# Performance work log

Measured on AMD Instinct MI355X. Metric: run time of the kernel, lower is better.

Reference implementation:

```python
import jax, jax.numpy as jnp
import numpy as np
import math

N_HEAD = 16
N_KV_HEAD = 4
N_EMBED = 2048
HEAD_DIM = N_EMBED // N_HEAD  # 128
ROPE_BASE = 10000.0


def _rope_tables(T, dim, dtype):
    inv_freq = 1.0 / (ROPE_BASE ** (jnp.arange(0, dim, 2, dtype=jnp.float32) / dim))
    t = jnp.arange(T, dtype=jnp.float32)
    freqs = jnp.outer(t, inv_freq)            # (T, dim/2)
    emb = jnp.concatenate([freqs, freqs], -1) # (T, dim)
    return jnp.cos(emb).astype(dtype), jnp.sin(emb).astype(dtype)


def _rotate_half(x):
    half = x.shape[-1] // 2
    return jnp.concatenate([-x[..., half:], x[..., :half]], axis=-1)


def setup_inputs() -> dict:
    key = jax.random.key(0)
    kx, kq, kk, kv, ko = jax.random.split(key, 5)
    B, T, C = 2, 2048, N_EMBED
    s = 0.02
    return {
        "x": jax.random.normal(kx, (B, T, C), jnp.float32),
        "Wq": jax.random.normal(kq, (N_HEAD * HEAD_DIM, C), jnp.float32) * s,
        "Wk": jax.random.normal(kk, (N_KV_HEAD * HEAD_DIM, C), jnp.float32) * s,
        "Wv": jax.random.normal(kv, (N_KV_HEAD * HEAD_DIM, C), jnp.float32) * s,
        "Wo": jax.random.normal(ko, (C, N_HEAD * HEAD_DIM), jnp.float32) * s,
    }


def reference(x, Wq, Wk, Wv, Wo):
    B, T, C = x.shape
    H, KV, D = N_HEAD, N_KV_HEAD, HEAD_DIM
    rep = H // KV

    q = jnp.einsum('btc,oc->bto', x, Wq).reshape(B, T, H, D).transpose(0, 2, 1, 3)   # (B,H,T,D)
    k = jnp.einsum('btc,oc->bto', x, Wk).reshape(B, T, KV, D).transpose(0, 2, 1, 3)  # (B,KV,T,D)
    v = jnp.einsum('btc,oc->bto', x, Wv).reshape(B, T, KV, D).transpose(0, 2, 1, 3)

    cos, sin = _rope_tables(T, D, x.dtype)  # (T,D) broadcast over (B,h,T,D)
    q = q * cos + _rotate_half(q) * sin
    k = k * cos + _rotate_half(k) * sin

    # GQA: head h attends to kv head h // rep (== repeat_interleave in torch).
    qg = q.reshape(B, KV, rep, T, D)
    scale = 1.0 / math.sqrt(D)
    attn = jnp.einsum('bgrtd,bgsd->bgrts', qg, k) * scale  # (B,KV,rep,T,T)
    causal = jnp.tril(jnp.ones((T, T), dtype=bool))
    attn = jnp.where(causal, attn, -jnp.inf)
    attn = jax.nn.softmax(attn, axis=-1)
    out = jnp.einsum('bgrts,bgsd->bgrtd', attn, v)          # (B,KV,rep,T,D)
    out = out.reshape(B, H, T, D).transpose(0, 2, 1, 3).reshape(B, T, H * D)
    return jnp.einsum('bto,co->btc', out, Wo)
```

## Files before the change

### kernel.cpp

```cpp
#include <hip/hip_runtime.h>
#include <stdint.h>

typedef unsigned short u16;
typedef __attribute__((ext_vector_type(8))) short short8;
typedef __attribute__((ext_vector_type(4))) short short4v;
typedef __attribute__((ext_vector_type(4))) float f32x4;

#define NB_  2
#define NT_  2048
#define NC_  2048
#define NH_  16
#define NKV_ 4
#define HD_  128
#define NM_  (NB_*NT_)
#define NQKV 3072

__device__ __forceinline__ u16 f2b(float x) {
  uint32_t u = __float_as_uint(x);
  u += 0x7fffu + ((u >> 16) & 1u);
  return (u16)(u >> 16);
}
__device__ __forceinline__ float b2f(u16 x) {
  return __uint_as_float(((uint32_t)x) << 16);
}
__device__ __forceinline__ uint32_t pk2t(float a, float b) {
  return (__float_as_uint(a) >> 16) | (__float_as_uint(b) & 0xFFFF0000u);
}

typedef __attribute__((address_space(1))) uint32_t* gp1_t;
typedef __attribute__((address_space(3))) uint32_t* lp3_t;
__device__ __forceinline__ void async_ld16(const void* g, void* l) {
  __builtin_amdgcn_global_load_lds((gp1_t)(uintptr_t)g, (lp3_t)(uintptr_t)l, 16, 0, 0);
}

__global__ void f2bf_all(const float* __restrict__ x,  const float* __restrict__ wq,
                         const float* __restrict__ wk, const float* __restrict__ wv,
                         const float* __restrict__ wo,
                         u16* xb, u16* wqb, u16* wkb, u16* wvb, u16* wob) {
  int bid = blockIdx.x;
  const float* src; u16* dst; int base;
  if      (bid < 8192)  { src = x;  dst = xb;  base = bid; }
  else if (bid < 12288) { src = wq; dst = wqb; base = bid - 8192; }
  else if (bid < 13312) { src = wk; dst = wkb; base = bid - 12288; }
  else if (bid < 14336) { src = wv; dst = wvb; base = bid - 13312; }
  else                  { src = wo; dst = wob; base = bid - 14336; }
  int i = base * 256 + threadIdx.x;
  const float4 v = ((const float4*)src)[i];
  short4v o;
  o[0] = (short)f2b(v.x); o[1] = (short)f2b(v.y);
  o[2] = (short)f2b(v.z); o[3] = (short)f2b(v.w);
  *(short4v*)(dst + (size_t)i * 4) = o;
}

__global__ void postk(const u16* __restrict__ qkv,
                      u16* __restrict__ Qr, u16* __restrict__ Kr, u16* __restrict__ Vt) {
  __shared__ u16 tile[64][72];
  int bid = blockIdx.x;
  if (bid < 20480) {
    u16* out; int nheads; int tid; int coff; float osc;
    if (bid < 16384) { out = Qr; nheads = NH_;  tid = bid * 256 + threadIdx.x; coff = 0;
                       osc = 0.08838834764831845f; }
    else             { out = Kr; nheads = NKV_; tid = (bid - 16384) * 256 + threadIdx.x; coff = 2048;
                       osc = 1.0f; }
    int j = tid & 63;
    int t = (tid >> 6) & (NT_ - 1);
    int bh = tid >> 17;
    int h = bh % nheads, b = bh / nheads;
    const u16* src = qkv + ((size_t)(b * NT_ + t)) * NQKV + coff + h * HD_;
    float q0 = b2f(src[j]), q1 = b2f(src[j + 64]);
    float inv = expf(-0.14391156831212787f * (float)j);
    float ang = (float)t * inv;
    float c = cosf(ang), s = sinf(ang);
    u16* dst = out + ((size_t)(b * nheads + h) * NT_ + t) * HD_;
    dst[j]      = f2b((q0 * c - q1 * s) * osc);
    dst[j + 64] = f2b((q1 * c + q0 * s) * osc);
  } else {
    int idx = bid - 20480;
    int tt = idx & 63, dd = idx >> 6;
    int tid = threadIdx.x;
    int r = tid >> 3, c8 = (tid & 7) * 8;
#pragma unroll
    for (int it = 0; it < 2; ++it) {
      int row = r + it * 32;
      short8 v = *(const short8*)(qkv + (size_t)(tt * 64 + row) * NQKV + 2560 + dd * 64 + c8);
      *(short8*)(&tile[row][c8]) = v;
    }
    __syncthreads();
    int b = (tt * 64) >> 11, t0 = (tt * 64) & (NT_ - 1);
    int dl = tid >> 3, t8 = (tid & 7) * 8;
#pragma unroll
    for (int it = 0; it < 2; ++it) {
      int d = dl + it * 32;
      int gcol = dd * 64 + d;
      int kv = gcol >> 7, drow = gcol & 127;
      short8 v;
#pragma unroll
      for (int k = 0; k < 8; ++k) v[k] = (short)tile[t8 + k][d];
      *(short8*)(Vt + ((size_t)(b * NKV_ + kv) * HD_ + drow) * NT_ + t0 + t8) = v;
    }
  }
}

__global__ __launch_bounds__(256, 2)
void gemm192(const u16* __restrict__ A, const u16* __restrict__ B, u16* __restrict__ C, int K)
{
  __shared__ u16 As[2 * 128 * 32];
  __shared__ u16 Bs[2 * 192 * 32];
  const int bx = blockIdx.x, by = blockIdx.y;
  const int m0 = by * 128, n0 = bx * 192;
  const int tid = threadIdx.x;
  const int wave = tid >> 6, lane = tid & 63;
  const int quad = lane >> 4, l15 = lane & 15;
  const int wm = wave >> 1, wn = wave & 1;

  const int p_local = lane >> 3;
  const int s7 = lane & 7;
  const int mlo = s7 >> 2;
  const int gg = (s7 & 3) ^ (p_local & 3);
  const int rowc = p_local * 2 + mlo;
  const int kel = gg * 8;

  const u16* Ag[2]; u16* Al[2];
#pragma unroll
  for (int q = 0; q < 2; ++q) {
    const int c = wave * 2 + q;
    Ag[q] = A + (size_t)(m0 + c * 16 + rowc) * K + kel;
    Al[q] = As + c * 512;
  }
  const u16* Bg[3]; u16* Bl[3];
#pragma unroll
  for (int q = 0; q < 3; ++q) {
    const int c = wave * 3 + q;
    Bg[q] = B + (size_t)(n0 + c * 16 + rowc) * K + kel;
    Bl[q] = Bs + c * 512;
  }

  f32x4 acc[4][6] = {};

  int a_addr[4], b_addr[6];
#pragma unroll
  for (int i = 0; i < 4; ++i) {
    int m = wm * 64 + i * 16 + l15;
    a_addr[i] = ((m >> 1) * 8 + (m & 1) * 4 + (quad ^ ((m >> 1) & 3))) * 8;
  }
#pragma unroll
  for (int i = 0; i < 6; ++i) {
    int n = wn * 96 + i * 16 + l15;
    b_addr[i] = ((n >> 1) * 8 + (n & 1) * 4 + (quad ^ ((n >> 1) & 3))) * 8;
  }

  const int nk = K >> 5;
#pragma unroll
  for (int q = 0; q < 2; ++q) async_ld16(Ag[q], Al[q]);
#pragma unroll
  for (int q = 0; q < 3; ++q) async_ld16(Bg[q], Bl[q]);

  for (int i = 0; i < nk; ++i) {
    __syncthreads();
    if (i + 1 < nk) {
      const int offA = ((i + 1) & 1) * 4096;
      const int offB = ((i + 1) & 1) * 6144;
      const int k0 = (i + 1) << 5;
#pragma unroll
      for (int q = 0; q < 2; ++q) async_ld16(Ag[q] + k0, Al[q] + offA);
#pragma unroll
      for (int q = 0; q < 3; ++q) async_ld16(Bg[q] + k0, Bl[q] + offB);
    }
    const int offA = (i & 1) * 4096;
    const int offB = (i & 1) * 6144;
    short8 af[4], bf[6];
#pragma unroll
    for (int j = 0; j < 4; ++j) af[j] = *(const short8*)(As + offA + a_addr[j]);
#pragma unroll
    for (int j = 0; j < 6; ++j) bf[j] = *(const short8*)(Bs + offB + b_addr[j]);
#pragma unroll
    for (int mb = 0; mb < 4; ++mb)
#pragma unroll
      for (int nb = 0; nb < 6; ++nb)
        acc[mb][nb] = __builtin_amdgcn_mfma_f32_16x16x32_bf16(af[mb], bf[nb], acc[mb][nb], 0, 0, 0);
  }

#pragma unroll
  for (int mb = 0; mb < 4; ++mb)
#pragma unroll
    for (int nb = 0; nb < 6; ++nb) {
      const int gn = n0 + wn * 96 + nb * 16 + l15;
#pragma unroll
      for (int r = 0; r < 4; ++r) {
        const int gm = m0 + wm * 64 + mb * 16 + quad * 4 + r;
        C[(size_t)gm * NQKV + gn] = f2b(acc[mb][nb][r]);
      }
    }
}

__global__ __launch_bounds__(256, 2)
void gemm128o(const u16* __restrict__ A, const u16* __restrict__ B, float* __restrict__ C, int K)
{
  __shared__ u16 As[2 * 128 * 32];
  __shared__ u16 Bs[2 * 128 * 32];
  const int bx = blockIdx.x, by = blockIdx.y;
  const int m0 = by * 128, n0 = bx * 128;
  const int tid = threadIdx.x;
  const int wave = tid >> 6, lane = tid & 63;
  const int quad = lane >> 4, l15 = lane & 15;
  const int wm = wave >> 1, wn = wave & 1;

  const int p_local = lane >> 3;
  const int s7 = lane & 7;
  const int mlo = s7 >> 2;
  const int gg = (s7 & 3) ^ (p_local & 3);
  const int rowc = p_local * 2 + mlo;
  const int kel = gg * 8;

  const u16* Ag[2]; const u16* Bg[2];
  u16* Al[2]; u16* Bl[2];
#pragma unroll
  for (int q = 0; q < 2; ++q) {
    const int c = wave * 2 + q;
    Ag[q] = A + (size_t)(m0 + c * 16 + rowc) * K + kel;
    Bg[q] = B + (size_t)(n0 + c * 16 + rowc) * K + kel;
    Al[q] = As + c * 512;
    Bl[q] = Bs + c * 512;
  }

  f32x4 acc[4][4] = {};

  int a_addr[4], b_addr[4];
#pragma unroll
  for (int i = 0; i < 4; ++i) {
    int m = wm * 64 + i * 16 + l15;
    a_addr[i] = ((m >> 1) * 8 + (m & 1) * 4 + (quad ^ ((m >> 1) & 3))) * 8;
    int n = wn * 64 + i * 16 + l15;
    b_addr[i] = ((n >> 1) * 8 + (n & 1) * 4 + (quad ^ ((n >> 1) & 3))) * 8;
  }

  const int nk = K >> 5;
#pragma unroll
  for (int q = 0; q < 2; ++q) {
    async_ld16(Ag[q], Al[q]);
    async_ld16(Bg[q], Bl[q]);
  }

  for (int i = 0; i < nk; ++i) {
    __syncthreads();
    if (i + 1 < nk) {
      const int off = ((i + 1) & 1) * 4096;
      const int k0 = (i + 1) << 5;
#pragma unroll
      for (int q = 0; q < 2; ++q) {
        async_ld16(Ag[q] + k0, Al[q] + off);
        async_ld16(Bg[q] + k0, Bl[q] + off);
      }
    }
    const int off = (i & 1) * 4096;
    short8 af[4], bf[4];
#pragma unroll
    for (int j = 0; j < 4; ++j) af[j] = *(const short8*)(As + off + a_addr[j]);
#pragma unroll
    for (int j = 0; j < 4; ++j) bf[j] = *(const short8*)(Bs + off + b_addr[j]);
#pragma unroll
    for (int mb = 0; mb < 4; ++mb)
#pragma unroll
      for (int nb = 0; nb < 4; ++nb)
        acc[mb][nb] = __builtin_amdgcn_mfma_f32_16x16x32_bf16(af[mb], bf[nb], acc[mb][nb], 0, 0, 0);
  }

#pragma unroll
  for (int mb = 0; mb < 4; ++mb)
#pragma unroll
    for (int nb = 0; nb < 4; ++nb) {
      const int gn = n0 + wn * 64 + nb * 16 + l15;
#pragma unroll
      for (int r = 0; r < 4; ++r) {
        const int gm = m0 + wm * 64 + mb * 16 + quad * 4 + r;
        C[(size_t)gm * NC_ + gn] = acc[mb][nb][r];
      }
    }
}

__global__ __launch_bounds__(256, 2)
void attn_kernel(const u16* __restrict__ Q, const u16* __restrict__ Kg,
                 const u16* __restrict__ Vt, u16* __restrict__ O)
{
  __shared__ u16 Ks[2 * 8192];
  __shared__ u16 Vs[2 * 8192];
  const int bx = blockIdx.x;
  const int h  = blockIdx.y;
  const int b  = blockIdx.z;
  const int qi = b ? (15 - bx) : bx;
  const int kv = h >> 2;
  const int tid = threadIdx.x;
  const int wave = tid >> 6, lane = tid & 63;
  const int quad = lane >> 4, l15 = lane & 15;
  const int qw = qi * 128 + wave * 32;

  const u16* Kbase = Kg + (size_t)(b * NKV_ + kv) * NT_ * HD_;
  const u16* Vbase = Vt + (size_t)(b * NKV_ + kv) * HD_ * NT_;

  short8 qf[2][4];
#pragma unroll
  for (int qs = 0; qs < 2; ++qs) {
    const u16* qb = Q + ((size_t)(b * NH_ + h) * NT_ + qw + qs * 16 + l15) * HD_ + quad * 8;
#pragma unroll
    for (int kb = 0; kb < 4; ++kb) qf[qs][kb] = *(const short8*)(qb + kb * 32);
  }

  const int krow = lane >> 4, kgs = lane & 15;
  const int vrow = lane >> 3, vgs = lane & 7;

  auto stage = [&](int kt, int pbuf) {
    u16* KsB = Ks + pbuf * 8192;
    u16* VsB = Vs + pbuf * 8192;
#pragma unroll
    for (int qq = 0; qq < 4; ++qq) {
      const int c = wave * 4 + qq;
      const int rk = c * 4 + krow;
      const int gk = kgs ^ (rk & 7);
      async_ld16(Kbase + (size_t)(kt * 64 + rk) * HD_ + gk * 8, KsB + c * 512);
      const int rv = c * 8 + vrow;
      const int gv = vgs ^ (rv & 7);
      async_ld16(Vbase + (size_t)rv * NT_ + kt * 64 + gv * 8, VsB + c * 512);
    }
  };

  short8 vone;
#pragma unroll
  for (int j = 0; j < 8; ++j) vone[j] = (short)0x3F80;

  f32x4 acc_o[2][8] = {};
  f32x4 acc_l[2] = {};
  const int nkt = 2 * qi + 2;

  stage(0, 0);

  for (int kt = 0; kt < nkt; ++kt) {
    __syncthreads();
    if (kt + 1 < nkt) stage(kt + 1, (kt + 1) & 1);
    if (kt * 64 > qw + 31) continue;

    const u16* KsB = Ks + (kt & 1) * 8192;
    const u16* VsB = Vs + (kt & 1) * 8192;

    f32x4 S[2][4] = {};
#pragma unroll
    for (int nb = 0; nb < 4; ++nb) {
      const int row = nb * 16 + l15;
#pragma unroll
      for (int kb = 0; kb < 4; ++kb) {
        const int gi = kb * 4 + quad;
        short8 kfr = *(const short8*)(KsB + row * 128 + (gi ^ (row & 7)) * 8);
        S[0][nb] = __builtin_amdgcn_mfma_f32_16x16x32_bf16(kfr, qf[0][kb], S[0][nb], 0, 0, 0);
        S[1][nb] = __builtin_amdgcn_mfma_f32_16x16x32_bf16(kfr, qf[1][kb], S[1][nb], 0, 0, 0);
      }
    }

#pragma unroll
    for (int qs = 0; qs < 2; ++qs) {
      if (kt * 64 + 63 > qw + qs * 16) {
        const int qg = qw + qs * 16 + l15;
#pragma unroll
        for (int nb = 0; nb < 4; ++nb)
#pragma unroll
          for (int r = 0; r < 4; ++r) {
            const int key = kt * 64 + nb * 16 + quad * 4 + r;
            if (key > qg) S[qs][nb][r] = -INFINITY;
          }
      }
    }

#pragma unroll
    for (int qs = 0; qs < 2; ++qs)
#pragma unroll
      for (int nb = 0; nb < 4; ++nb)
#pragma unroll
        for (int r = 0; r < 4; ++r)
          S[qs][nb][r] = __expf(S[qs][nb][r]);

    short8 pf[2][2];
#pragma unroll
    for (int qs = 0; qs < 2; ++qs) {
      uint32_t d0[4], d1[4];
#pragma unroll
      for (int nb = 0; nb < 4; ++nb) {
        d0[nb] = pk2t(S[qs][nb][0], S[qs][nb][1]);
        d1[nb] = pk2t(S[qs][nb][2], S[qs][nb][3]);
      }
      const int srcA = ((quad & 1) * 2) * 16 + l15;
      const int srcB = srcA + 16;
      const bool hi = quad >= 2;
#pragma unroll
      for (int k2 = 0; k2 < 2; ++k2) {
        const int nbL = k2 * 2, nbH = k2 * 2 + 1;
        uint32_t a0 = (uint32_t)__shfl((int)d0[nbL], srcA);
        uint32_t a1 = (uint32_t)__shfl((int)d1[nbL], srcA);
        uint32_t a2 = (uint32_t)__shfl((int)d0[nbL], srcB);
        uint32_t a3 = (uint32_t)__shfl((int)d1[nbL], srcB);
        uint32_t b0 = (uint32_t)__shfl((int)d0[nbH], srcA);
        uint32_t b1 = (uint32_t)__shfl((int)d1[nbH], srcA);
        uint32_t b2 = (uint32_t)__shfl((int)d0[nbH], srcB);
        uint32_t b3 = (uint32_t)__shfl((int)d1[nbH], srcB);
        uint32_t w[4] = { hi ? b0 : a0, hi ? b1 : a1, hi ? b2 : a2, hi ? b3 : a3 };
        pf[qs][k2] = *(short8*)w;
      }
    }

#pragma unroll
    for (int qs = 0; qs < 2; ++qs) {
      acc_l[qs] = __builtin_amdgcn_mfma_f32_16x16x32_bf16(pf[qs][0], vone, acc_l[qs], 0, 0, 0);
      acc_l[qs] = __builtin_amdgcn_mfma_f32_16x16x32_bf16(pf[qs][1], vone, acc_l[qs], 0, 0, 0);
    }

#pragma unroll
    for (int db = 0; db < 8; ++db) {
      const int row = db * 16 + l15;
#pragma unroll
      for (int k2 = 0; k2 < 2; ++k2) {
        const int gi = k2 * 4 + quad;
        short8 vf = *(const short8*)(VsB + row * 64 + (gi ^ (row & 7)) * 8);
        acc_o[0][db] = __builtin_amdgcn_mfma_f32_16x16x32_bf16(pf[0][k2], vf, acc_o[0][db], 0, 0, 0);
        acc_o[1][db] = __builtin_amdgcn_mfma_f32_16x16x32_bf16(pf[1][k2], vf, acc_o[1][db], 0, 0, 0);
      }
    }
  }

#pragma unroll
  for (int qs = 0; qs < 2; ++qs) {
    float inv_r[4];
#pragma unroll
    for (int r = 0; r < 4; ++r) inv_r[r] = 1.f / acc_l[qs][r];
    const size_t orow = ((size_t)b * NT_ + qw + qs * 16) * (NH_ * HD_);
#pragma unroll
    for (int db = 0; db < 8; ++db)
#pragma unroll
      for (int r = 0; r < 4; ++r)
        O[orow + (size_t)(quad * 4 + r) * (NH_ * HD_) + h * HD_ + db * 16 + l15] =
            f2b(acc_o[qs][db][r] * inv_r[r]);
  }
}

extern "C" void kernel_launch(void* const* d_in, const int* in_sizes, int n_in,
                              void* d_out, int out_size, void* d_ws, size_t ws_size,
                              hipStream_t stream) {
  const float* x  = (const float*)d_in[0];
  const float* Wq = (const float*)d_in[1];
  const float* Wk = (const float*)d_in[2];
  const float* Wv = (const float*)d_in[3];
  const float* Wo = (const float*)d_in[4];
  float* out = (float*)d_out;
  char* ws = (char*)d_ws;
  const size_t MB = (size_t)1 << 20;
  u16* xb    = (u16*)(ws + 0);
  u16* wqkv  = (u16*)(ws + 16 * MB);
  u16* wkb   = (u16*)(ws + 24 * MB);
  u16* wvb   = (u16*)(ws + 26 * MB);
  u16* wob   = (u16*)(ws + 28 * MB);
  u16* qkvrw = (u16*)(ws + 36 * MB);
  u16* Qr    = (u16*)(ws + 60 * MB);
  u16* Kr    = (u16*)(ws + 76 * MB);
  u16* Vtb   = (u16*)(ws + 80 * MB);
  u16* Ob    = xb;

  f2bf_all<<<18432, 256, 0, stream>>>(x, Wq, Wk, Wv, Wo, xb, wqkv, wkb, wvb, wob);

  gemm192<<<dim3(16, 32), 256, 0, stream>>>(xb, wqkv, qkvrw, 2048);

  postk<<<20992, 256, 0, stream>>>(qkvrw, Qr, Kr, Vtb);

  attn_kernel<<<dim3(16, 16, 2), 256, 0, stream>>>(Qr, Kr, Vtb, Ob);

  gemm128o<<<dim3(16, 32), 256, 0, stream>>>(Ob, wob, out, 2048);
}
```

Baseline: 283.7 us.

## Split attention work across 8 waves with 16 query rows each

The attention kernel now launches 512 threads per block, and each of the 8 waves handles 16 query rows instead of 32. This halves per-wave accumulator registers so more waves can be resident, and it halves the K/V staging each wave does. MFMA sections are also wrapped in s_setprio to favour matrix issue. In exchange, each K fragment read from LDS now feeds only one MFMA instead of two, which raises LDS traffic per unit of compute.

```diff
diff --git a/kernel.cpp b/kernel.cpp
--- a/kernel.cpp
+++ b/kernel.cpp
@@ -278,7 +278,7 @@
     }
 }
 
-__global__ __launch_bounds__(256, 2)
+__global__ __launch_bounds__(512, 4)
 void attn_kernel(const u16* __restrict__ Q, const u16* __restrict__ Kg,
                  const u16* __restrict__ Vt, u16* __restrict__ O)
 {
@@ -292,17 +292,16 @@
   const int tid = threadIdx.x;
   const int wave = tid >> 6, lane = tid & 63;
   const int quad = lane >> 4, l15 = lane & 15;
-  const int qw = qi * 128 + wave * 32;
+  const int qw = qi * 128 + wave * 16;
 
   const u16* Kbase = Kg + (size_t)(b * NKV_ + kv) * NT_ * HD_;
   const u16* Vbase = Vt + (size_t)(b * NKV_ + kv) * HD_ * NT_;
 
-  short8 qf[2][4];
-#pragma unroll
-  for (int qs = 0; qs < 2; ++qs) {
-    const u16* qb = Q + ((size_t)(b * NH_ + h) * NT_ + qw + qs * 16 + l15) * HD_ + quad * 8;
-#pragma unroll
-    for (int kb = 0; kb < 4; ++kb) qf[qs][kb] = *(const short8*)(qb + kb * 32);
+  short8 qf[4];
+  {
+    const u16* qb = Q + ((size_t)(b * NH_ + h) * NT_ + qw + l15) * HD_ + quad * 8;
+#pragma unroll
+    for (int kb = 0; kb < 4; ++kb) qf[kb] = *(const short8*)(qb + kb * 32);
   }
 
   const int krow = lane >> 4, kgs = lane & 15;
@@ -312,8 +311,8 @@
     u16* KsB = Ks + pbuf * 8192;
     u16* VsB = Vs + pbuf * 8192;
 #pragma unroll
-    for (int qq = 0; qq < 4; ++qq) {
-      const int c = wave * 4 + qq;
+    for (int qq = 0; qq < 2; ++qq) {
+      const int c = wave * 2 + qq;
       const int rk = c * 4 + krow;
       const int gk = kgs ^ (rk & 7);
       async_ld16(Kbase + (size_t)(kt * 64 + rk) * HD_ + gk * 8, KsB + c * 512);
@@ -327,8 +326,8 @@
 #pragma unroll
   for (int j = 0; j < 8; ++j) vone[j] = (short)0x3F80;
 
-  f32x4 acc_o[2][8] = {};
-  f32x4 acc_l[2] = {};
+  f32x4 acc_o[8] = {};
+  f32x4 acc_l = {};
   const int nkt = 2 * qi + 2;
 
   stage(0, 0);
@@ -336,12 +335,13 @@
   for (int kt = 0; kt < nkt; ++kt) {
     __syncthreads();
     if (kt + 1 < nkt) stage(kt + 1, (kt + 1) & 1);
-    if (kt * 64 > qw + 31) continue;
+    if (kt * 64 > qw + 15) continue;
 
     const u16* KsB = Ks + (kt & 1) * 8192;
     const u16* VsB = Vs + (kt & 1) * 8192;
 
-    f32x4 S[2][4] = {};
+    f32x4 S[4] = {};
+    __builtin_amdgcn_s_setprio(1);
 #pragma unroll
     for (int nb = 0; nb < 4; ++nb) {
       const int row = nb * 16 + l15;
@@ -349,41 +349,35 @@
       for (int kb = 0; kb < 4; ++kb) {
         const int gi = kb * 4 + quad;
         short8 kfr = *(const short8*)(KsB + row * 128 + (gi ^ (row & 7)) * 8);
-        S[0][nb] = __builtin_amdgcn_mfma_f32_16x16x32_bf16(kfr, qf[0][kb], S[0][nb], 0, 0, 0);
-        S[1][nb] = __builtin_amdgcn_mfma_f32_16x16x32_bf16(kfr, qf[1][kb], S[1][nb], 0, 0, 0);
-      }
-    }
-
-#pragma unroll
-    for (int qs = 0; qs < 2; ++qs) {
-      if (kt * 64 + 63 > qw + qs * 16) {
-        const int qg = qw + qs * 16 + l15;
-#pragma unroll
-        for (int nb = 0; nb < 4; ++nb)
-#pragma unroll
-          for (int r = 0; r < 4; ++r) {
-            const int key = kt * 64 + nb * 16 + quad * 4 + r;
-            if (key > qg) S[qs][nb][r] = -INFINITY;
-          }
-      }
-    }
-
-#pragma unroll
-    for (int qs = 0; qs < 2; ++qs)
+        S[nb] = __builtin_amdgcn_mfma_f32_16x16x32_bf16(kfr, qf[kb], S[nb], 0, 0, 0);
+      }
+    }
+    __builtin_amdgcn_s_setprio(0);
+
+    if (kt * 64 + 63 > qw) {
+      const int qg = qw + l15;
 #pragma unroll
       for (int nb = 0; nb < 4; ++nb)
 #pragma unroll
-        for (int r = 0; r < 4; ++r)
-          S[qs][nb][r] = __expf(S[qs][nb][r]);
-
-    short8 pf[2][2];
-#pragma unroll
-    for (int qs = 0; qs < 2; ++qs) {
+        for (int r = 0; r < 4; ++r) {
+          const int key = kt * 64 + nb * 16 + quad * 4 + r;
+          if (key > qg) S[nb][r] = -INFINITY;
+        }
+    }
+
+#pragma unroll
+    for (int nb = 0; nb < 4; ++nb)
+#pragma unroll
+      for (int r = 0; r < 4; ++r)
+        S[nb][r] = __expf(S[nb][r]);
+
+    short8 pf[2];
+    {
       uint32_t d0[4], d1[4];
 #pragma unroll
       for (int nb = 0; nb < 4; ++nb) {
-        d0[nb] = pk2t(S[qs][nb][0], S[qs][nb][1]);
-        d1[nb] = pk2t(S[qs][nb][2], S[qs][nb][3]);
+        d0[nb] = pk2t(S[nb][0], S[nb][1]);
+        d1[nb] = pk2t(S[nb][2], S[nb][3]);
       }
       const int srcA = ((quad & 1) * 2) * 16 + l15;
       const int srcB = srcA + 16;
@@ -400,16 +394,14 @@
         uint32_t b2 = (uint32_t)__shfl((int)d0[nbH], srcB);
         uint32_t b3 = (uint32_t)__shfl((int)d1[nbH], srcB);
         uint32_t w[4] = { hi ? b0 : a0, hi ? b1 : a1, hi ? b2 : a2, hi ? b3 : a3 };
-        pf[qs][k2] = *(short8*)w;
-      }
-    }
-
-#pragma unroll
-    for (int qs = 0; qs < 2; ++qs) {
-      acc_l[qs] = __builtin_amdgcn_mfma_f32_16x16x32_bf16(pf[qs][0], vone, acc_l[qs], 0, 0, 0);
-      acc_l[qs] = __builtin_amdgcn_mfma_f32_16x16x32_bf16(pf[qs][1], vone, acc_l[qs], 0, 0, 0);
-    }
-
+        pf[k2] = *(short8*)w;
+      }
+    }
+
+    acc_l = __builtin_amdgcn_mfma_f32_16x16x32_bf16(pf[0], vone, acc_l, 0, 0, 0);
+    acc_l = __builtin_amdgcn_mfma_f32_16x16x32_bf16(pf[1], vone, acc_l, 0, 0, 0);
+
+    __builtin_amdgcn_s_setprio(1);
 #pragma unroll
     for (int db = 0; db < 8; ++db) {
       const int row = db * 16 + l15;
@@ -417,24 +409,23 @@
       for (int k2 = 0; k2 < 2; ++k2) {
         const int gi = k2 * 4 + quad;
         short8 vf = *(const short8*)(VsB + row * 64 + (gi ^ (row & 7)) * 8);
-        acc_o[0][db] = __builtin_amdgcn_mfma_f32_16x16x32_bf16(pf[0][k2], vf, acc_o[0][db], 0, 0, 0);
-        acc_o[1][db] = __builtin_amdgcn_mfma_f32_16x16x32_bf16(pf[1][k2], vf, acc_o[1][db], 0, 0, 0);
-      }
-    }
-  }
-
-#pragma unroll
-  for (int qs = 0; qs < 2; ++qs) {
+        acc_o[db] = __builtin_amdgcn_mfma_f32_16x16x32_bf16(pf[k2], vf, acc_o[db], 0, 0, 0);
+      }
+    }
+    __builtin_amdgcn_s_setprio(0);
+  }
+
+  {
     float inv_r[4];
 #pragma unroll
-    for (int r = 0; r < 4; ++r) inv_r[r] = 1.f / acc_l[qs][r];
-    const size_t orow = ((size_t)b * NT_ + qw + qs * 16) * (NH_ * HD_);
+    for (int r = 0; r < 4; ++r) inv_r[r] = 1.f / acc_l[r];
+    const size_t orow = ((size_t)b * NT_ + qw) * (NH_ * HD_);
 #pragma unroll
     for (int db = 0; db < 8; ++db)
 #pragma unroll
       for (int r = 0; r < 4; ++r)
         O[orow + (size_t)(quad * 4 + r) * (NH_ * HD_) + h * HD_ + db * 16 + l15] =
-            f2b(acc_o[qs][db][r] * inv_r[r]);
+            f2b(acc_o[db][r] * inv_r[r]);
   }
 }
 
@@ -466,7 +457,7 @@
 
   postk<<<20992, 256, 0, stream>>>(qkvrw, Qr, Kr, Vtb);
 
-  attn_kernel<<<dim3(16, 16, 2), 256, 0, stream>>>(Qr, Kr, Vtb, Ob);
+  attn_kernel<<<dim3(16, 16, 2), 512, 0, stream>>>(Qr, Kr, Vtb, Ob);
 
   gemm128o<<<dim3(16, 32), 256, 0, stream>>>(Ob, wob, out, 2048);
 }
```

Result: no change. 285.9 us (+0.8%).

## Split attention key tiles across wave pairs and precompute RoPE cos/sin table

Applied to the files above, without the earlier changes.

The attention kernel now runs 512 threads per block. Each pair of waves shares a 32-row query slice and splits every 64-key tile into two 32-key halves, and the partial O and row-sum accumulators are merged through shared memory at the end. MFMA sections are wrapped in s_setprio hints. RoPE cos/sin values are computed once into a table by extra blocks of the conversion kernel and then read in postk, so the transcendental math is no longer repeated per head. This should raise wave-level parallelism and latency hiding in attention, at the cost of an extra reduction step, more barriers, and one more table read.

```diff
diff --git a/kernel.cpp b/kernel.cpp
--- a/kernel.cpp
+++ b/kernel.cpp
@@ -36,8 +36,17 @@
 __global__ void f2bf_all(const float* __restrict__ x,  const float* __restrict__ wq,
                          const float* __restrict__ wk, const float* __restrict__ wv,
                          const float* __restrict__ wo,
-                         u16* xb, u16* wqb, u16* wkb, u16* wvb, u16* wob) {
+                         u16* xb, u16* wqb, u16* wkb, u16* wvb, u16* wob,
+                         float2* __restrict__ tab) {
   int bid = blockIdx.x;
+  if (bid >= 18432) {
+    int idx = (bid - 18432) * 256 + threadIdx.x;
+    int t = idx >> 6, j = idx & 63;
+    float inv = expf(-0.14391156831212787f * (float)j);
+    float ang = (float)t * inv;
+    tab[idx] = make_float2(cosf(ang), sinf(ang));
+    return;
+  }
   const float* src; u16* dst; int base;
   if      (bid < 8192)  { src = x;  dst = xb;  base = bid; }
   else if (bid < 12288) { src = wq; dst = wqb; base = bid - 8192; }
@@ -52,7 +61,7 @@
   *(short4v*)(dst + (size_t)i * 4) = o;
 }
 
-__global__ void postk(const u16* __restrict__ qkv,
+__global__ void postk(const u16* __restrict__ qkv, const float2* __restrict__ tab,
                       u16* __restrict__ Qr, u16* __restrict__ Kr, u16* __restrict__ Vt) {
   __shared__ u16 tile[64][72];
   int bid = blockIdx.x;
@@ -68,9 +77,8 @@
     int h = bh % nheads, b = bh / nheads;
     const u16* src = qkv + ((size_t)(b * NT_ + t)) * NQKV + coff + h * HD_;
     float q0 = b2f(src[j]), q1 = b2f(src[j + 64]);
-    float inv = expf(-0.14391156831212787f * (float)j);
-    float ang = (float)t * inv;
-    float c = cosf(ang), s = sinf(ang);
+    float2 cs = tab[t * 64 + j];
+    float c = cs.x, s = cs.y;
     u16* dst = out + ((size_t)(b * nheads + h) * NT_ + t) * HD_;
     dst[j]      = f2b((q0 * c - q1 * s) * osc);
     dst[j + 64] = f2b((q1 * c + q0 * s) * osc);
@@ -278,12 +286,13 @@
     }
 }
 
-__global__ __launch_bounds__(256, 2)
+__global__ __launch_bounds__(512, 4)
 void attn_kernel(const u16* __restrict__ Q, const u16* __restrict__ Kg,
                  const u16* __restrict__ Vt, u16* __restrict__ O)
 {
-  __shared__ u16 Ks[2 * 8192];
-  __shared__ u16 Vs[2 * 8192];
+  __shared__ __align__(16) u16 smem[4 * 8192];
+  u16* Ks = smem;
+  u16* Vs = smem + 2 * 8192;
   const int bx = blockIdx.x;
   const int h  = blockIdx.y;
   const int b  = blockIdx.z;
@@ -292,7 +301,8 @@
   const int tid = threadIdx.x;
   const int wave = tid >> 6, lane = tid & 63;
   const int quad = lane >> 4, l15 = lane & 15;
-  const int qw = qi * 128 + wave * 32;
+  const int pair = wave >> 1, half = wave & 1;
+  const int qw = qi * 128 + pair * 32;
 
   const u16* Kbase = Kg + (size_t)(b * NKV_ + kv) * NT_ * HD_;
   const u16* Vbase = Vt + (size_t)(b * NKV_ + kv) * HD_ * NT_;
@@ -312,8 +322,8 @@
     u16* KsB = Ks + pbuf * 8192;
     u16* VsB = Vs + pbuf * 8192;
 #pragma unroll
-    for (int qq = 0; qq < 4; ++qq) {
-      const int c = wave * 4 + qq;
+    for (int qq = 0; qq < 2; ++qq) {
+      const int c = wave * 2 + qq;
       const int rk = c * 4 + krow;
       const int gk = kgs ^ (rk & 7);
       async_ld16(Kbase + (size_t)(kt * 64 + rk) * HD_ + gk * 8, KsB + c * 512);
@@ -336,15 +346,17 @@
   for (int kt = 0; kt < nkt; ++kt) {
     __syncthreads();
     if (kt + 1 < nkt) stage(kt + 1, (kt + 1) & 1);
-    if (kt * 64 > qw + 31) continue;
+    const int k0 = kt * 64 + half * 32;
+    if (k0 > qw + 31) continue;
 
     const u16* KsB = Ks + (kt & 1) * 8192;
     const u16* VsB = Vs + (kt & 1) * 8192;
 
-    f32x4 S[2][4] = {};
-#pragma unroll
-    for (int nb = 0; nb < 4; ++nb) {
-      const int row = nb * 16 + l15;
+    f32x4 S[2][2] = {};
+    __builtin_amdgcn_s_setprio(1);
+#pragma unroll
+    for (int nb = 0; nb < 2; ++nb) {
+      const int row = half * 32 + nb * 16 + l15;
 #pragma unroll
       for (int kb = 0; kb < 4; ++kb) {
         const int gi = kb * 4 + quad;
@@ -353,16 +365,17 @@
         S[1][nb] = __builtin_amdgcn_mfma_f32_16x16x32_bf16(kfr, qf[1][kb], S[1][nb], 0, 0, 0);
       }
     }
+    __builtin_amdgcn_s_setprio(0);
 
 #pragma unroll
     for (int qs = 0; qs < 2; ++qs) {
-      if (kt * 64 + 63 > qw + qs * 16) {
+      if (k0 + 31 > qw + qs * 16) {
         const int qg = qw + qs * 16 + l15;
 #pragma unroll
-        for (int nb = 0; nb < 4; ++nb)
+        for (int nb = 0; nb < 2; ++nb)
 #pragma unroll
           for (int r = 0; r < 4; ++r) {
-            const int key = kt * 64 + nb * 16 + quad * 4 + r;
+            const int key = k0 + nb * 16 + quad * 4 + r;
             if (key > qg) S[qs][nb][r] = -INFINITY;
           }
       }
@@ -371,70 +384,78 @@
 #pragma unroll
     for (int qs = 0; qs < 2; ++qs)
 #pragma unroll
-      for (int nb = 0; nb < 4; ++nb)
+      for (int nb = 0; nb < 2; ++nb)
 #pragma unroll
         for (int r = 0; r < 4; ++r)
           S[qs][nb][r] = __expf(S[qs][nb][r]);
 
-    short8 pf[2][2];
+    short8 pf[2];
 #pragma unroll
     for (int qs = 0; qs < 2; ++qs) {
-      uint32_t d0[4], d1[4];
-#pragma unroll
-      for (int nb = 0; nb < 4; ++nb) {
+      uint32_t d0[2], d1[2];
+#pragma unroll
+      for (int nb = 0; nb < 2; ++nb) {
         d0[nb] = pk2t(S[qs][nb][0], S[qs][nb][1]);
         d1[nb] = pk2t(S[qs][nb][2], S[qs][nb][3]);
       }
-      const int srcA = ((quad & 1) * 2) * 16 + l15;
+      const int srcA = (quad & 1) * 32 + l15;
       const int srcB = srcA + 16;
       const bool hi = quad >= 2;
-#pragma unroll
-      for (int k2 = 0; k2 < 2; ++k2) {
-        const int nbL = k2 * 2, nbH = k2 * 2 + 1;
-        uint32_t a0 = (uint32_t)__shfl((int)d0[nbL], srcA);
-        uint32_t a1 = (uint32_t)__shfl((int)d1[nbL], srcA);
-        uint32_t a2 = (uint32_t)__shfl((int)d0[nbL], srcB);
-        uint32_t a3 = (uint32_t)__shfl((int)d1[nbL], srcB);
-        uint32_t b0 = (uint32_t)__shfl((int)d0[nbH], srcA);
-        uint32_t b1 = (uint32_t)__shfl((int)d1[nbH], srcA);
-        uint32_t b2 = (uint32_t)__shfl((int)d0[nbH], srcB);
-        uint32_t b3 = (uint32_t)__shfl((int)d1[nbH], srcB);
-        uint32_t w[4] = { hi ? b0 : a0, hi ? b1 : a1, hi ? b2 : a2, hi ? b3 : a3 };
-        pf[qs][k2] = *(short8*)w;
-      }
-    }
-
-#pragma unroll
-    for (int qs = 0; qs < 2; ++qs) {
-      acc_l[qs] = __builtin_amdgcn_mfma_f32_16x16x32_bf16(pf[qs][0], vone, acc_l[qs], 0, 0, 0);
-      acc_l[qs] = __builtin_amdgcn_mfma_f32_16x16x32_bf16(pf[qs][1], vone, acc_l[qs], 0, 0, 0);
-    }
-
+      uint32_t a0 = (uint32_t)__shfl((int)d0[0], srcA);
+      uint32_t a1 = (uint32_t)__shfl((int)d1[0], srcA);
+      uint32_t a2 = (uint32_t)__shfl((int)d0[0], srcB);
+      uint32_t a3 = (uint32_t)__shfl((int)d1[0], srcB);
+      uint32_t b0 = (uint32_t)__shfl((int)d0[1], srcA);
+      uint32_t b1 = (uint32_t)__shfl((int)d1[1], srcA);
+      uint32_t b2 = (uint32_t)__shfl((int)d0[1], srcB);
+      uint32_t b3 = (uint32_t)__shfl((int)d1[1], srcB);
+      uint32_t w[4] = { hi ? b0 : a0, hi ? b1 : a1, hi ? b2 : a2, hi ? b3 : a3 };
+      pf[qs] = *(short8*)w;
+    }
+
+    acc_l[0] = __builtin_amdgcn_mfma_f32_16x16x32_bf16(pf[0], vone, acc_l[0], 0, 0, 0);
+    acc_l[1] = __builtin_amdgcn_mfma_f32_16x16x32_bf16(pf[1], vone, acc_l[1], 0, 0, 0);
+
+    __builtin_amdgcn_s_setprio(1);
 #pragma unroll
     for (int db = 0; db < 8; ++db) {
       const int row = db * 16 + l15;
-#pragma unroll
-      for (int k2 = 0; k2 < 2; ++k2) {
-        const int gi = k2 * 4 + quad;
-        short8 vf = *(const short8*)(VsB + row * 64 + (gi ^ (row & 7)) * 8);
-        acc_o[0][db] = __builtin_amdgcn_mfma_f32_16x16x32_bf16(pf[0][k2], vf, acc_o[0][db], 0, 0, 0);
-        acc_o[1][db] = __builtin_amdgcn_mfma_f32_16x16x32_bf16(pf[1][k2], vf, acc_o[1][db], 0, 0, 0);
-      }
-    }
-  }
-
+      const int gi = half * 4 + quad;
+      short8 vf = *(const short8*)(VsB + row * 64 + (gi ^ (row & 7)) * 8);
+      acc_o[0][db] = __builtin_amdgcn_mfma_f32_16x16x32_bf16(pf[0], vf, acc_o[0][db], 0, 0, 0);
+      acc_o[1][db] = __builtin_amdgcn_mfma_f32_16x16x32_bf16(pf[1], vf, acc_o[1][db], 0, 0, 0);
+    }
+    __builtin_amdgcn_s_setprio(0);
+  }
+
+  __syncthreads();
+  f32x4* shp = (f32x4*)smem;
 #pragma unroll
   for (int qs = 0; qs < 2; ++qs) {
-    float inv_r[4];
-#pragma unroll
-    for (int r = 0; r < 4; ++r) inv_r[r] = 1.f / acc_l[qs][r];
-    const size_t orow = ((size_t)b * NT_ + qw + qs * 16) * (NH_ * HD_);
-#pragma unroll
-    for (int db = 0; db < 8; ++db)
-#pragma unroll
-      for (int r = 0; r < 4; ++r)
-        O[orow + (size_t)(quad * 4 + r) * (NH_ * HD_) + h * HD_ + db * 16 + l15] =
-            f2b(acc_o[qs][db][r] * inv_r[r]);
+    if (half == 1) {
+      f32x4* dst = shp + (size_t)(pair * 64 + lane) * 9;
+#pragma unroll
+      for (int db = 0; db < 8; ++db) dst[db] = acc_o[qs][db];
+      dst[8] = acc_l[qs];
+    }
+    __syncthreads();
+    if (half == 0) {
+      const f32x4* src = shp + (size_t)(pair * 64 + lane) * 9;
+      f32x4 lsum = acc_l[qs] + src[8];
+      float inv_r[4];
+#pragma unroll
+      for (int r = 0; r < 4; ++r) inv_r[r] = 1.f / lsum[r];
+      const size_t orow = ((size_t)b * NT_ + qw + qs * 16) * (NH_ * HD_);
+#pragma unroll
+      for (int db = 0; db < 8; ++db) {
+        f32x4 osum = acc_o[qs][db] + src[db];
+#pragma unroll
+        for (int r = 0; r < 4; ++r)
+          O[orow + (size_t)(quad * 4 + r) * (NH_ * HD_) + h * HD_ + db * 16 + l15] =
+              f2b(osum[r] * inv_r[r]);
+      }
+    }
+    __syncthreads();
   }
 }
 
@@ -458,15 +479,16 @@
   u16* Qr    = (u16*)(ws + 60 * MB);
   u16* Kr    = (u16*)(ws + 76 * MB);
   u16* Vtb   = (u16*)(ws + 80 * MB);
+  float2* tab = (float2*)(ws + 84 * MB);
   u16* Ob    = xb;
 
-  f2bf_all<<<18432, 256, 0, stream>>>(x, Wq, Wk, Wv, Wo, xb, wqkv, wkb, wvb, wob);
+  f2bf_all<<<18944, 256, 0, stream>>>(x, Wq, Wk, Wv, Wo, xb, wqkv, wkb, wvb, wob, tab);
 
   gemm192<<<dim3(16, 32), 256, 0, stream>>>(xb, wqkv, qkvrw, 2048);
 
-  postk<<<20992, 256, 0, stream>>>(qkvrw, Qr, Kr, Vtb);
-
-  attn_kernel<<<dim3(16, 16, 2), 256, 0, stream>>>(Qr, Kr, Vtb, Ob);
+  postk<<<20992, 256, 0, stream>>>(qkvrw, tab, Qr, Kr, Vtb);
+
+  attn_kernel<<<dim3(16, 16, 2), 512, 0, stream>>>(Qr, Kr, Vtb, Ob);
 
   gemm128o<<<dim3(16, 32), 256, 0, stream>>>(Ob, wob, out, 2048);
 }
```

Measured after the change: 430.9 us. 1.52x slower.
